# Optimization experiments

Hardware: AMD Instinct MI355X
Metric: run time of the kernel (lower is better)

Reference implementation:

```python
import jax, jax.numpy as jnp
import numpy as np

EMB_SIZE = 50000
D = 256            # emb_dimension
TIMES = 3
D3 = D * TIMES     # 768
RESCALE = 20.0
BATCH = 128
NEG = 5


def setup_inputs() -> dict:
    key = jax.random.key(0)
    ks = jax.random.split(key, 12)
    initrange = 1.0 / D
    return {
        "pos_u": jax.random.randint(ks[0], (BATCH,), 0, EMB_SIZE),
        "pos_v": jax.random.randint(ks[1], (BATCH,), 0, EMB_SIZE),
        "neg_v": jax.random.randint(ks[2], (BATCH, NEG), 0, EMB_SIZE),
        "time": jax.random.uniform(ks[3], (BATCH,), dtype=jnp.float32) * RESCALE,
        "m1": jax.random.normal(ks[4], (1, D), dtype=jnp.float32) / jnp.sqrt(2.0),
        "b1": jax.random.normal(ks[5], (D,), dtype=jnp.float32) * 0.5,
        "W2": jax.random.normal(ks[6], (D, D), dtype=jnp.float32) / jnp.sqrt(D),   # dense2 weight (out,in)
        "b2": jnp.zeros((D,), dtype=jnp.float32),
        "W4": jax.random.normal(ks[7], (D3, D), dtype=jnp.float32) / jnp.sqrt(D),  # dense4 weight (out,in)
        "b4": jnp.zeros((D3,), dtype=jnp.float32),
        "U": jax.random.uniform(ks[8], (EMB_SIZE, D3), dtype=jnp.float32,
                                 minval=-initrange, maxval=initrange),
        "V": jax.random.uniform(ks[9], (EMB_SIZE, D3), dtype=jnp.float32,
                                 minval=-initrange, maxval=initrange),
        "T": jax.random.normal(ks[10], (D, D, D3), dtype=jnp.float32) / D,
        "B": jax.random.normal(ks[11], (D, D), dtype=jnp.float32) / D,
    }


def reference(pos_u, pos_v, neg_v, time, m1, b1, W2, b2, W4, b4, U, V, T, B):
    # time encoding: h1 = tanh(t/rescale * m1 + b1); timevec = tanh(dense2(h1))
    h1 = jnp.tanh((time[:, None] / RESCALE) * m1 + b1)          # (b, d)
    tv = jnp.tanh(h1 @ W2.T + b2)                               # (b, d)
    tvB = tv @ B                                                # einsum('bij,bi->bj') of broadcast B

    # positive target word: (T . emb_u + B) contracted with timevec, then dense4
    emb_u = U[pos_u]                                            # (b, 3d)
    h3_u = jnp.einsum('ijk,bk,bi->bj', T, emb_u, tv) + tvB      # (b, d)
    use_w = h3_u @ W4.T + b4                                    # (b, 3d)

    # positive context word
    emb_v = V[pos_v]                                            # (b, 3d)
    h3_v = jnp.einsum('ijk,bk,bi->bj', T, emb_v, tv) + tvB      # (b, d)
    use_c_v = h3_v @ W4.T + b4                                  # (b, 3d)

    # negative samples: fused contraction avoids the (b, l, d, d) intermediate
    emb_n = V[neg_v]                                            # (b, l, 3d)
    h3_n = jnp.einsum('ijk,blk,bi->blj', T, emb_n, tv) + tvB[:, None, :]  # (b, l, d)
    use_c_n = h3_n @ W4.T + b4                                  # (b, l, 3d)

    score = jnp.sum(use_w * use_c_v, axis=1)
    score = jnp.clip(score, -10.0, 10.0)
    score = -jax.nn.log_sigmoid(score)                          # (b,)

    neg_score = jnp.einsum('blk,bk->bl', use_c_n, use_w)        # bmm with use_w
    neg_score = jnp.clip(neg_score, -10.0, 10.0)
    neg_score = -jnp.mean(jax.nn.log_sigmoid(-neg_score), axis=1)  # (b,)

    return (jnp.mean(score + neg_score), jnp.mean(score), jnp.mean(neg_score))
```

## Files before the change

### kernel.cpp

```cpp
#include <hip/hip_runtime.h>
#include <hip/hip_bf16.h>

#define DD   256
#define DD3  768
#define NB   128
#define NE   7

#define OFF_TVT  0u
#define OFF_TVB  32768u
#define OFF_EMB  65536u
#define OFF_H3   753664u
#define OFF_G    983040u
#define OFF_GV   1048576u
#define OFF_SC   1048832u

typedef __attribute__((ext_vector_type(8))) short bf16x8;
typedef __attribute__((ext_vector_type(4))) float f32x4;

__device__ __forceinline__ unsigned bf16rne(float f) {
  unsigned u = __float_as_uint(f);
  return (u + 0x7fffu + ((u >> 16) & 1u)) >> 16;
}

__device__ __forceinline__ void gld16(const float* g, float* l) {
  __builtin_amdgcn_global_load_lds(
      (const __attribute__((address_space(1))) unsigned int*)g,
      (__attribute__((address_space(3))) unsigned int*)l, 16, 0, 0);
}

__global__ void k_setup(const float* __restrict__ timev,
                        const float* __restrict__ m1,
                        const float* __restrict__ b1,
                        const float* __restrict__ W2,
                        const float* __restrict__ b2,
                        const float* __restrict__ Bm,
                        float* __restrict__ tv_t,
                        float* __restrict__ tvB) {
  const int b = blockIdx.x, i = threadIdx.x;
  __shared__ float h1[DD];
  __shared__ float tvs[DD];
  const float t = timev[b] * (1.0f / 20.0f);
  h1[i] = tanhf(fmaf(t, m1[i], b1[i]));
  __syncthreads();
  float acc = b2[i];
  const float* w2r = W2 + i * DD;
#pragma unroll 8
  for (int jj = 0; jj < DD; ++jj) acc = fmaf(h1[jj], w2r[jj], acc);
  const float tvi = tanhf(acc);
  tvs[i] = tvi;
  tv_t[i * NB + b] = tvi;
  __syncthreads();
  float a2 = 0.f;
#pragma unroll 8
  for (int ii = 0; ii < DD; ++ii) a2 = fmaf(tvs[ii], Bm[ii * DD + i], a2);
  tvB[b * DD + i] = a2;
}

__global__ void k_pack(const float* __restrict__ tv_t, short* __restrict__ tvf) {
  const int t = blockIdx.x * 256 + threadIdx.x;
  const int f = t >> 6, l = t & 63;
  const int b = (f >> 3) * 16 + (l & 15);
  const int i0 = (f & 7) * 32 + ((l >> 4) & 3) * 8;
  bf16x8 v;
#pragma unroll
  for (int jj = 0; jj < 8; ++jj)
    v[jj] = (short)bf16rne(tv_t[(i0 + jj) * NB + b]);
  *(bf16x8*)(tvf + (long)t * 8) = v;
}

__global__ void k_gather(const int* __restrict__ pos_u,
                         const int* __restrict__ pos_v,
                         const int* __restrict__ neg_v,
                         const float* __restrict__ U,
                         const float* __restrict__ V,
                         float* __restrict__ emb) {
  const int be = blockIdx.x;
  const int b = be / NE, e = be % NE;
  const float* src;
  if (e == 0)      src = U + (long)pos_u[b] * DD3;
  else if (e == 1) src = V + (long)pos_v[b] * DD3;
  else             src = V + (long)neg_v[b * 5 + (e - 2)] * DD3;
  const float4 v = ((const float4*)src)[threadIdx.x];
  ((float4*)(emb + ((long)e * NB + b) * DD3))[threadIdx.x] = v;
}

__global__ __launch_bounds__(1024) void k_gram(const float* __restrict__ W4,
                                               const float* __restrict__ b4,
                                               float* __restrict__ G,
                                               float* __restrict__ gv) {
  const int p = blockIdx.x, t = threadIdx.x;
  const int q = t & 255, nq = t >> 8;
  __shared__ float colp[DD3];
  __shared__ float red[4][257];
  __shared__ float gred[4];
  for (int n = t; n < DD3; n += 1024) colp[n] = W4[n * DD + p];
  __syncthreads();
  float acc = 0.f;
  const int n0 = nq * 192;
#pragma unroll 8
  for (int n = n0; n < n0 + 192; ++n) acc = fmaf(colp[n], W4[n * DD + q], acc);
  red[nq][q] = acc;
  float gp = 0.f;
  for (int n = n0; n < n0 + 192; ++n) gp = fmaf(b4[n], colp[n], gp);
  if (q == 0) gred[nq] = gp;
  __syncthreads();
  if (t < 256) G[p * DD + t] = red[0][t] + red[1][t] + red[2][t] + red[3][t];
  if (t == 0) gv[p] = gred[0] + gred[1] + gred[2] + gred[3];
}

__global__ __launch_bounds__(512) void k_main(const float* __restrict__ T,
                                              const short* __restrict__ tvf,
                                              const float* __restrict__ emb,
                                              const float* __restrict__ tvB,
                                              float* __restrict__ h3) {
  __shared__ float Ts[2][4096];
  __shared__ float h3red[NB][NE];
  const int t = threadIdx.x;
  const int j = blockIdx.x;
  const int l = t & 63;
  const int w = t >> 6;
  const int bq = w >> 1;
  const int mh = w & 1;
  const int l15 = l & 15;
  const int l4 = (l >> 4) & 3;
  const int lhi = l >> 5;
  const int kb = (l & 31) * 4;

  bf16x8 tvfr[2][8];
#pragma unroll
  for (int nf = 0; nf < 2; ++nf)
#pragma unroll
    for (int it = 0; it < 8; ++it)
      tvfr[nf][it] = *(const bf16x8*)(tvf + ((((bq * 2 + nf) * 8) + it) * 64 + l) * 8);

  const int i0 = 4 * w + lhi, i1 = i0 + 2;
  const float* gp0 = T + (long)i0 * 196608 + j * 768 + (kb ^ (((i0 >> 3) & 3) << 4));
  const float* gp1 = T + (long)i1 * 196608 + j * 768 + (kb ^ (((i1 >> 3) & 3) << 4));

  auto stage = [&](int kcp, int itp, int bufp) {
    const long o = (long)itp * 6291456 + kcp * 128;
    gld16(gp0 + o, &Ts[bufp][(w * 2 + 0) * 256]);
    gld16(gp1 + o, &Ts[bufp][(w * 2 + 1) * 256]);
  };

  float h3p[NE][2];
#pragma unroll
  for (int e = 0; e < NE; ++e) { h3p[e][0] = 0.f; h3p[e][1] = 0.f; }

  stage(0, 0, 0);
  const int kcol0 = mh * 64;

#pragma unroll 1
  for (int kc = 0; kc < 6; ++kc) {
    f32x4 acc[4][2];
#pragma unroll
    for (int mf = 0; mf < 4; ++mf) {
      acc[mf][0] = {0.f, 0.f, 0.f, 0.f};
      acc[mf][1] = {0.f, 0.f, 0.f, 0.f};
    }
#pragma unroll
    for (int it = 0; it < 8; ++it) {
      if (it < 7) {
        stage(kc, it + 1, (it + 1) & 1);
        asm volatile("s_waitcnt vmcnt(2)" ::: "memory");
      } else if (kc < 5) {
        stage(kc + 1, 0, 0);
        asm volatile("s_waitcnt vmcnt(2)" ::: "memory");
      } else {
        asm volatile("s_waitcnt vmcnt(0)" ::: "memory");
      }
      __builtin_amdgcn_s_barrier();
      asm volatile("" ::: "memory");
      const float* tsb = &Ts[it & 1][0];
#pragma unroll
      for (int mf = 0; mf < 4; ++mf) {
        const int kx = (kcol0 + mf * 16 + l15) ^ (l4 << 4);
        bf16x8 af;
#pragma unroll
        for (int jj = 0; jj < 8; ++jj)
          af[jj] = (short)bf16rne(tsb[(l4 * 8 + jj) * 128 + kx]);
        acc[mf][0] = __builtin_amdgcn_mfma_f32_16x16x32_bf16(af, tvfr[0][it], acc[mf][0], 0, 0, 0);
        acc[mf][1] = __builtin_amdgcn_mfma_f32_16x16x32_bf16(af, tvfr[1][it], acc[mf][1], 0, 0, 0);
      }
      asm volatile("" ::: "memory");
      __builtin_amdgcn_s_barrier();
      asm volatile("" ::: "memory");
    }
#pragma unroll
    for (int nf = 0; nf < 2; ++nf) {
      const int b = bq * 32 + nf * 16 + l15;
#pragma unroll
      for (int mf = 0; mf < 4; ++mf) {
        const long ko = (long)kc * 128 + mh * 64 + mf * 16 + l4 * 4;
#pragma unroll
        for (int e = 0; e < NE; ++e) {
          const f32x4 em = *(const f32x4*)(emb + ((long)e * NB + b) * 768 + ko);
          float s = h3p[e][nf];
          s = fmaf(acc[mf][nf][0], em[0], s);
          s = fmaf(acc[mf][nf][1], em[1], s);
          s = fmaf(acc[mf][nf][2], em[2], s);
          s = fmaf(acc[mf][nf][3], em[3], s);
          h3p[e][nf] = s;
        }
      }
    }
  }

  float hr[NE][2];
#pragma unroll
  for (int e = 0; e < NE; ++e)
#pragma unroll
    for (int nf = 0; nf < 2; ++nf) {
      float v = h3p[e][nf];
      v += __shfl_xor(v, 16);
      v += __shfl_xor(v, 32);
      hr[e][nf] = v;
    }
  __syncthreads();
  if (mh == 0 && l < 16) {
#pragma unroll
    for (int e = 0; e < NE; ++e) {
      h3red[bq * 32 + l][e]      = hr[e][0];
      h3red[bq * 32 + 16 + l][e] = hr[e][1];
    }
  }
  __syncthreads();
  if (mh == 1 && l < 16) {
#pragma unroll
    for (int nf = 0; nf < 2; ++nf) {
      const int b = bq * 32 + nf * 16 + l;
      const float tb = tvB[b * DD + j];
#pragma unroll
      for (int e = 0; e < NE; ++e)
        h3[((long)b * NE + e) * DD + j] = h3red[b][e] + hr[e][nf] + tb;
    }
  }
}

__global__ void k_score(const float* __restrict__ h3,
                        const float* __restrict__ G,
                        const float* __restrict__ gv,
                        const float* __restrict__ b4,
                        float* __restrict__ scoreb,
                        float* __restrict__ negb) {
  const int b = blockIdx.x, t = threadIdx.x;
  __shared__ float h3s[NE * DD];
  __shared__ float red[4][16];
  for (int idx = t; idx < NE * DD; idx += 256) h3s[idx] = h3[(long)b * NE * DD + idx];
  __syncthreads();
  float racc = 0.f;
#pragma unroll 8
  for (int jp = 0; jp < DD; ++jp) racc = fmaf(G[jp * DD + t], h3s[jp], racc);

  float loc[14];
#pragma unroll
  for (int e = 1; e < NE; ++e) loc[e - 1] = racc * h3s[e * DD + t];
  loc[6] = gv[t] * h3s[t];
#pragma unroll
  for (int e = 1; e < NE; ++e) loc[6 + e] = gv[t] * h3s[e * DD + t];
  loc[13] = b4[t] * b4[t] + b4[t + 256] * b4[t + 256] + b4[t + 512] * b4[t + 512];

  const int lane = t & 63, wid = t >> 6;
#pragma unroll
  for (int qd = 0; qd < 14; ++qd) {
    float v = loc[qd];
#pragma unroll
    for (int m = 1; m < 64; m <<= 1) v += __shfl_xor(v, m);
    if (lane == 0) red[wid][qd] = v;
  }
  __syncthreads();
  if (t == 0) {
    float r[14];
#pragma unroll
    for (int qd = 0; qd < 14; ++qd)
      r[qd] = red[0][qd] + red[1][qd] + red[2][qd] + red[3][qd];
    const float c = r[13], gu = r[6];
    auto logsig = [](float x) { return fminf(x, 0.f) - log1pf(expf(-fabsf(x))); };
    float dv = r[0] + gu + r[7] + c;
    dv = fminf(fmaxf(dv, -10.f), 10.f);
    const float sc = -logsig(dv);
    float ns = 0.f;
    for (int lx = 1; lx < 6; ++lx) {
      float dn = r[lx] + gu + r[7 + lx] + c;
      dn = fminf(fmaxf(dn, -10.f), 10.f);
      ns -= logsig(-dn);
    }
    scoreb[b] = sc;
    negb[b] = ns * 0.2f;
  }
}

__global__ void k_final(const float* __restrict__ scoreb,
                        const float* __restrict__ negb,
                        float* __restrict__ out) {
  const int t = threadIdx.x;
  float s = scoreb[t], n = negb[t];
#pragma unroll
  for (int m = 1; m < 64; m <<= 1) {
    s += __shfl_xor(s, m);
    n += __shfl_xor(n, m);
  }
  __shared__ float rs[2], rn[2];
  if ((t & 63) == 0) { rs[t >> 6] = s; rn[t >> 6] = n; }
  __syncthreads();
  if (t == 0) {
    const float S = (rs[0] + rs[1]) * (1.0f / 128.0f);
    const float N = (rn[0] + rn[1]) * (1.0f / 128.0f);
    out[0] = S + N;
    out[1] = S;
    out[2] = N;
  }
}

extern "C" void kernel_launch(void* const* d_in, const int* in_sizes, int n_in,
                              void* d_out, int out_size, void* d_ws, size_t ws_size,
                              hipStream_t stream) {
  const int*   pos_u = (const int*)d_in[0];
  const int*   pos_v = (const int*)d_in[1];
  const int*   neg_v = (const int*)d_in[2];
  const float* timev = (const float*)d_in[3];
  const float* m1    = (const float*)d_in[4];
  const float* b1    = (const float*)d_in[5];
  const float* W2    = (const float*)d_in[6];
  const float* b2    = (const float*)d_in[7];
  const float* W4    = (const float*)d_in[8];
  const float* b4    = (const float*)d_in[9];
  const float* U     = (const float*)d_in[10];
  const float* V     = (const float*)d_in[11];
  const float* T     = (const float*)d_in[12];
  const float* Bm    = (const float*)d_in[13];

  float* ws     = (float*)d_ws;
  float* tv_t   = ws + OFF_TVT;
  float* tvB    = ws + OFF_TVB;
  float* emb    = ws + OFF_EMB;
  float* h3     = ws + OFF_H3;
  float* G      = ws + OFF_G;
  float* gv     = ws + OFF_GV;
  short* tvf    = (short*)(ws + OFF_SC);
  float* scoreb = ws + OFF_SC;
  float* negb   = ws + OFF_SC + 128;
  float* out    = (float*)d_out;

  k_setup<<<128, 256, 0, stream>>>(timev, m1, b1, W2, b2, Bm, tv_t, tvB);
  k_pack<<<16, 256, 0, stream>>>(tv_t, tvf);
  k_gather<<<896, 192, 0, stream>>>(pos_u, pos_v, neg_v, U, V, emb);
  k_gram<<<256, 1024, 0, stream>>>(W4, b4, G, gv);
  k_main<<<256, 512, 0, stream>>>(T, tvf, emb, tvB, h3);
  k_score<<<128, 256, 0, stream>>>(h3, G, gv, b4, scoreb, negb);
  k_final<<<1, 128, 0, stream>>>(scoreb, negb, out);
}
```

Before: 182.5 us.

## Split k_main over batch halves with XCD-aware mapping and deeper staging

k_main now launches 512 blocks. Each block handles one output column j and half of the batch, and block ids are remapped so that blocks sharing a column land on the same XCD and can share L2. The T-slice staging ring grows from 2 to 4 LDS buffers with 3 stages in flight, and MFMA sections are wrapped in s_setprio. The aim is more parallelism and better latency hiding on the T stream. The cost is that each T slice is now read by two blocks instead of one, and LDS use per block rises.

```diff
diff --git a/kernel.cpp b/kernel.cpp
--- a/kernel.cpp
+++ b/kernel.cpp
@@ -113,10 +113,14 @@
                                               const float* __restrict__ emb,
                                               const float* __restrict__ tvB,
                                               float* __restrict__ h3) {
-  __shared__ float Ts[2][4096];
-  __shared__ float h3red[NB][NE];
+  __shared__ float Ts[4][4096];
+  __shared__ float h3red[64][NE];
+  const int bid = blockIdx.x;
+  const int xcd = bid & 7, slot = bid >> 3;
+  const int j = xcd * 32 + (slot >> 1);
+  const int bh = slot & 1;
+
   const int t = threadIdx.x;
-  const int j = blockIdx.x;
   const int l = t & 63;
   const int w = t >> 6;
   const int bq = w >> 1;
@@ -126,114 +130,129 @@
   const int lhi = l >> 5;
   const int kb = (l & 31) * 4;
 
-  bf16x8 tvfr[2][8];
-#pragma unroll
-  for (int nf = 0; nf < 2; ++nf)
-#pragma unroll
-    for (int it = 0; it < 8; ++it)
-      tvfr[nf][it] = *(const bf16x8*)(tvf + ((((bq * 2 + nf) * 8) + it) * 64 + l) * 8);
+  const int bf = bh * 4 + bq;
+  bf16x8 tvfr[8];
+#pragma unroll
+  for (int it = 0; it < 8; ++it)
+    tvfr[it] = *(const bf16x8*)(tvf + (((bf * 8) + it) * 64 + l) * 8);
 
   const int i0 = 4 * w + lhi, i1 = i0 + 2;
   const float* gp0 = T + (long)i0 * 196608 + j * 768 + (kb ^ (((i0 >> 3) & 3) << 4));
   const float* gp1 = T + (long)i1 * 196608 + j * 768 + (kb ^ (((i1 >> 3) & 3) << 4));
 
-  auto stage = [&](int kcp, int itp, int bufp) {
+  auto stage = [&](int sid) {
+    const int itp = sid & 7, kcp = sid >> 3, bufp = sid & 3;
     const long o = (long)itp * 6291456 + kcp * 128;
     gld16(gp0 + o, &Ts[bufp][(w * 2 + 0) * 256]);
     gld16(gp1 + o, &Ts[bufp][(w * 2 + 1) * 256]);
   };
 
-  float h3p[NE][2];
-#pragma unroll
-  for (int e = 0; e < NE; ++e) { h3p[e][0] = 0.f; h3p[e][1] = 0.f; }
-
-  stage(0, 0, 0);
+  float h3p[NE];
+#pragma unroll
+  for (int e = 0; e < NE; ++e) h3p[e] = 0.f;
+
   const int kcol0 = mh * 64;
 
+  auto compute = [&](int buf, int it, f32x4 (&acc)[4]) {
+    const float* tsb = &Ts[buf][0];
+    __builtin_amdgcn_s_setprio(1);
+#pragma unroll
+    for (int mf = 0; mf < 4; ++mf) {
+      const int kx = (kcol0 + mf * 16 + l15) ^ (l4 << 4);
+      bf16x8 af;
+#pragma unroll
+      for (int jj = 0; jj < 8; ++jj)
+        af[jj] = (short)bf16rne(tsb[(l4 * 8 + jj) * 128 + kx]);
+      acc[mf] = __builtin_amdgcn_mfma_f32_16x16x32_bf16(af, tvfr[it], acc[mf], 0, 0, 0);
+    }
+    __builtin_amdgcn_s_setprio(0);
+  };
+
+  auto epilogue = [&](int kc, f32x4 (&acc)[4]) {
+    const int b = bh * 64 + bq * 16 + l15;
+#pragma unroll
+    for (int mf = 0; mf < 4; ++mf) {
+      const long ko = (long)kc * 128 + mh * 64 + mf * 16 + l4 * 4;
+#pragma unroll
+      for (int e = 0; e < NE; ++e) {
+        const f32x4 em = *(const f32x4*)(emb + ((long)e * NB + b) * 768 + ko);
+        float s = h3p[e];
+        s = fmaf(acc[mf][0], em[0], s);
+        s = fmaf(acc[mf][1], em[1], s);
+        s = fmaf(acc[mf][2], em[2], s);
+        s = fmaf(acc[mf][3], em[3], s);
+        h3p[e] = s;
+      }
+    }
+  };
+
+  stage(0); stage(1); stage(2);
+
 #pragma unroll 1
-  for (int kc = 0; kc < 6; ++kc) {
-    f32x4 acc[4][2];
-#pragma unroll
-    for (int mf = 0; mf < 4; ++mf) {
-      acc[mf][0] = {0.f, 0.f, 0.f, 0.f};
-      acc[mf][1] = {0.f, 0.f, 0.f, 0.f};
-    }
+  for (int kc = 0; kc < 5; ++kc) {
+    f32x4 acc[4];
+#pragma unroll
+    for (int mf = 0; mf < 4; ++mf) acc[mf] = {0.f, 0.f, 0.f, 0.f};
 #pragma unroll
     for (int it = 0; it < 8; ++it) {
-      if (it < 7) {
-        stage(kc, it + 1, (it + 1) & 1);
-        asm volatile("s_waitcnt vmcnt(2)" ::: "memory");
-      } else if (kc < 5) {
-        stage(kc + 1, 0, 0);
+      const int sid = kc * 8 + it;
+      stage(sid + 3);
+      asm volatile("s_waitcnt vmcnt(6)" ::: "memory");
+      __builtin_amdgcn_s_barrier();
+      asm volatile("" ::: "memory");
+      compute(sid & 3, it, acc);
+      asm volatile("" ::: "memory");
+      __builtin_amdgcn_s_barrier();
+    }
+    epilogue(kc, acc);
+  }
+  {
+    f32x4 acc[4];
+#pragma unroll
+    for (int mf = 0; mf < 4; ++mf) acc[mf] = {0.f, 0.f, 0.f, 0.f};
+#pragma unroll
+    for (int it = 0; it < 8; ++it) {
+      const int sid = 40 + it;
+      if (it < 5) {
+        stage(sid + 3);
+        asm volatile("s_waitcnt vmcnt(6)" ::: "memory");
+      } else if (it == 5) {
+        asm volatile("s_waitcnt vmcnt(4)" ::: "memory");
+      } else if (it == 6) {
         asm volatile("s_waitcnt vmcnt(2)" ::: "memory");
       } else {
         asm volatile("s_waitcnt vmcnt(0)" ::: "memory");
       }
       __builtin_amdgcn_s_barrier();
       asm volatile("" ::: "memory");
-      const float* tsb = &Ts[it & 1][0];
-#pragma unroll
-      for (int mf = 0; mf < 4; ++mf) {
-        const int kx = (kcol0 + mf * 16 + l15) ^ (l4 << 4);
-        bf16x8 af;
-#pragma unroll
-        for (int jj = 0; jj < 8; ++jj)
-          af[jj] = (short)bf16rne(tsb[(l4 * 8 + jj) * 128 + kx]);
-        acc[mf][0] = __builtin_amdgcn_mfma_f32_16x16x32_bf16(af, tvfr[0][it], acc[mf][0], 0, 0, 0);
-        acc[mf][1] = __builtin_amdgcn_mfma_f32_16x16x32_bf16(af, tvfr[1][it], acc[mf][1], 0, 0, 0);
-      }
+      compute(sid & 3, it, acc);
       asm volatile("" ::: "memory");
       __builtin_amdgcn_s_barrier();
-      asm volatile("" ::: "memory");
-    }
-#pragma unroll
-    for (int nf = 0; nf < 2; ++nf) {
-      const int b = bq * 32 + nf * 16 + l15;
-#pragma unroll
-      for (int mf = 0; mf < 4; ++mf) {
-        const long ko = (long)kc * 128 + mh * 64 + mf * 16 + l4 * 4;
-#pragma unroll
-        for (int e = 0; e < NE; ++e) {
-          const f32x4 em = *(const f32x4*)(emb + ((long)e * NB + b) * 768 + ko);
-          float s = h3p[e][nf];
-          s = fmaf(acc[mf][nf][0], em[0], s);
-          s = fmaf(acc[mf][nf][1], em[1], s);
-          s = fmaf(acc[mf][nf][2], em[2], s);
-          s = fmaf(acc[mf][nf][3], em[3], s);
-          h3p[e][nf] = s;
-        }
-      }
-    }
-  }
-
-  float hr[NE][2];
-#pragma unroll
-  for (int e = 0; e < NE; ++e)
-#pragma unroll
-    for (int nf = 0; nf < 2; ++nf) {
-      float v = h3p[e][nf];
-      v += __shfl_xor(v, 16);
-      v += __shfl_xor(v, 32);
-      hr[e][nf] = v;
-    }
+    }
+    epilogue(5, acc);
+  }
+
+  float hr[NE];
+#pragma unroll
+  for (int e = 0; e < NE; ++e) {
+    float v = h3p[e];
+    v += __shfl_xor(v, 16);
+    v += __shfl_xor(v, 32);
+    hr[e] = v;
+  }
   __syncthreads();
   if (mh == 0 && l < 16) {
 #pragma unroll
-    for (int e = 0; e < NE; ++e) {
-      h3red[bq * 32 + l][e]      = hr[e][0];
-      h3red[bq * 32 + 16 + l][e] = hr[e][1];
-    }
+    for (int e = 0; e < NE; ++e) h3red[bq * 16 + l][e] = hr[e];
   }
   __syncthreads();
   if (mh == 1 && l < 16) {
-#pragma unroll
-    for (int nf = 0; nf < 2; ++nf) {
-      const int b = bq * 32 + nf * 16 + l;
-      const float tb = tvB[b * DD + j];
-#pragma unroll
-      for (int e = 0; e < NE; ++e)
-        h3[((long)b * NE + e) * DD + j] = h3red[b][e] + hr[e][nf] + tb;
-    }
+    const int bl = bq * 16 + l;
+    const int b = bh * 64 + bl;
+    const float tb = tvB[b * DD + j];
+#pragma unroll
+    for (int e = 0; e < NE; ++e)
+      h3[((long)b * NE + e) * DD + j] = h3red[bl][e] + hr[e] + tb;
   }
 }
 
@@ -346,7 +365,7 @@
   k_pack<<<16, 256, 0, stream>>>(tv_t, tvf);
   k_gather<<<896, 192, 0, stream>>>(pos_u, pos_v, neg_v, U, V, emb);
   k_gram<<<256, 1024, 0, stream>>>(W4, b4, G, gv);
-  k_main<<<256, 512, 0, stream>>>(T, tvf, emb, tvB, h3);
+  k_main<<<512, 512, 0, stream>>>(T, tvf, emb, tvB, h3);
   k_score<<<128, 256, 0, stream>>>(h3, G, gv, b4, scoreb, negb);
   k_final<<<1, 128, 0, stream>>>(scoreb, negb, out);
 }
```

Result: slower. 213.4 us (+16.9%).

## Split k_main over k-chunks across blocks with atomic reduction and triple buffering

Applied to the files above, without the earlier changes.

The k-chunk loop in k_main becomes a grid dimension, so 1536 blocks each handle one 128-wide k slice instead of 256 blocks looping over six. This raises parallelism across the MI355X CUs for the large T-streaming contraction. Partial h3 results are combined with atomicAdd into a buffer zeroed by a hipMemsetAsync, and tvB is added only by the kc==0 block. The kernel also switches to a three-stage LDS prefetch pipeline, raises MFMA wave priority with s_setprio, and adds a min-blocks launch bound. The costs are atomic contention, an extra memset launch, nondeterministic float summation order, and more LDS per block.

```diff
diff --git a/kernel.cpp b/kernel.cpp
--- a/kernel.cpp
+++ b/kernel.cpp
@@ -108,15 +108,18 @@
   if (t == 0) gv[p] = gred[0] + gred[1] + gred[2] + gred[3];
 }
 
-__global__ __launch_bounds__(512) void k_main(const float* __restrict__ T,
-                                              const short* __restrict__ tvf,
-                                              const float* __restrict__ emb,
-                                              const float* __restrict__ tvB,
-                                              float* __restrict__ h3) {
-  __shared__ float Ts[2][4096];
+__global__ __launch_bounds__(512, 4) void k_main(const float* __restrict__ T,
+                                                 const short* __restrict__ tvf,
+                                                 const float* __restrict__ emb,
+                                                 const float* __restrict__ tvB,
+                                                 float* __restrict__ h3) {
+  __shared__ float Ts[3][4096];
   __shared__ float h3red[NB][NE];
+  const int bid = blockIdx.x;
+  const int j = bid & 255;
+  const int kc = bid >> 8;
+
   const int t = threadIdx.x;
-  const int j = blockIdx.x;
   const int l = t & 63;
   const int w = t >> 6;
   const int bq = w >> 1;
@@ -134,74 +137,75 @@
       tvfr[nf][it] = *(const bf16x8*)(tvf + ((((bq * 2 + nf) * 8) + it) * 64 + l) * 8);
 
   const int i0 = 4 * w + lhi, i1 = i0 + 2;
-  const float* gp0 = T + (long)i0 * 196608 + j * 768 + (kb ^ (((i0 >> 3) & 3) << 4));
-  const float* gp1 = T + (long)i1 * 196608 + j * 768 + (kb ^ (((i1 >> 3) & 3) << 4));
-
-  auto stage = [&](int kcp, int itp, int bufp) {
-    const long o = (long)itp * 6291456 + kcp * 128;
-    gld16(gp0 + o, &Ts[bufp][(w * 2 + 0) * 256]);
-    gld16(gp1 + o, &Ts[bufp][(w * 2 + 1) * 256]);
+  const float* gp0 = T + (long)i0 * 196608 + j * 768 + kc * 128 + (kb ^ (((i0 >> 3) & 3) << 4));
+  const float* gp1 = T + (long)i1 * 196608 + j * 768 + kc * 128 + (kb ^ (((i1 >> 3) & 3) << 4));
+
+  auto stage = [&](int it) {
+    const int buf = it % 3;
+    const long o = (long)it * 6291456;
+    gld16(gp0 + o, &Ts[buf][(w * 2 + 0) * 256]);
+    gld16(gp1 + o, &Ts[buf][(w * 2 + 1) * 256]);
   };
 
+  const int kcol0 = mh * 64;
+
+  f32x4 acc[4][2];
+#pragma unroll
+  for (int mf = 0; mf < 4; ++mf) {
+    acc[mf][0] = {0.f, 0.f, 0.f, 0.f};
+    acc[mf][1] = {0.f, 0.f, 0.f, 0.f};
+  }
+
+  stage(0); stage(1);
+
+#pragma unroll
+  for (int it = 0; it < 8; ++it) {
+    if (it < 6) {
+      stage(it + 2);
+      asm volatile("s_waitcnt vmcnt(4)" ::: "memory");
+    } else if (it == 6) {
+      asm volatile("s_waitcnt vmcnt(2)" ::: "memory");
+    } else {
+      asm volatile("s_waitcnt vmcnt(0)" ::: "memory");
+    }
+    __builtin_amdgcn_s_barrier();
+    asm volatile("" ::: "memory");
+    const float* tsb = &Ts[it % 3][0];
+    __builtin_amdgcn_s_setprio(1);
+#pragma unroll
+    for (int mf = 0; mf < 4; ++mf) {
+      const int kx = (kcol0 + mf * 16 + l15) ^ (l4 << 4);
+      bf16x8 af;
+#pragma unroll
+      for (int jj = 0; jj < 8; ++jj)
+        af[jj] = (short)bf16rne(tsb[(l4 * 8 + jj) * 128 + kx]);
+      acc[mf][0] = __builtin_amdgcn_mfma_f32_16x16x32_bf16(af, tvfr[0][it], acc[mf][0], 0, 0, 0);
+      acc[mf][1] = __builtin_amdgcn_mfma_f32_16x16x32_bf16(af, tvfr[1][it], acc[mf][1], 0, 0, 0);
+    }
+    __builtin_amdgcn_s_setprio(0);
+    asm volatile("" ::: "memory");
+    __builtin_amdgcn_s_barrier();
+    asm volatile("" ::: "memory");
+  }
+
   float h3p[NE][2];
 #pragma unroll
   for (int e = 0; e < NE; ++e) { h3p[e][0] = 0.f; h3p[e][1] = 0.f; }
-
-  stage(0, 0, 0);
-  const int kcol0 = mh * 64;
-
-#pragma unroll 1
-  for (int kc = 0; kc < 6; ++kc) {
-    f32x4 acc[4][2];
+#pragma unroll
+  for (int nf = 0; nf < 2; ++nf) {
+    const int b = bq * 32 + nf * 16 + l15;
 #pragma unroll
     for (int mf = 0; mf < 4; ++mf) {
-      acc[mf][0] = {0.f, 0.f, 0.f, 0.f};
-      acc[mf][1] = {0.f, 0.f, 0.f, 0.f};
-    }
-#pragma unroll
-    for (int it = 0; it < 8; ++it) {
-      if (it < 7) {
-        stage(kc, it + 1, (it + 1) & 1);
-        asm volatile("s_waitcnt vmcnt(2)" ::: "memory");
-      } else if (kc < 5) {
-        stage(kc + 1, 0, 0);
-        asm volatile("s_waitcnt vmcnt(2)" ::: "memory");
-      } else {
-        asm volatile("s_waitcnt vmcnt(0)" ::: "memory");
-      }
-      __builtin_amdgcn_s_barrier();
-      asm volatile("" ::: "memory");
-      const float* tsb = &Ts[it & 1][0];
-#pragma unroll
-      for (int mf = 0; mf < 4; ++mf) {
-        const int kx = (kcol0 + mf * 16 + l15) ^ (l4 << 4);
-        bf16x8 af;
-#pragma unroll
-        for (int jj = 0; jj < 8; ++jj)
-          af[jj] = (short)bf16rne(tsb[(l4 * 8 + jj) * 128 + kx]);
-        acc[mf][0] = __builtin_amdgcn_mfma_f32_16x16x32_bf16(af, tvfr[0][it], acc[mf][0], 0, 0, 0);
-        acc[mf][1] = __builtin_amdgcn_mfma_f32_16x16x32_bf16(af, tvfr[1][it], acc[mf][1], 0, 0, 0);
-      }
-      asm volatile("" ::: "memory");
-      __builtin_amdgcn_s_barrier();
-      asm volatile("" ::: "memory");
-    }
-#pragma unroll
-    for (int nf = 0; nf < 2; ++nf) {
-      const int b = bq * 32 + nf * 16 + l15;
-#pragma unroll
-      for (int mf = 0; mf < 4; ++mf) {
-        const long ko = (long)kc * 128 + mh * 64 + mf * 16 + l4 * 4;
-#pragma unroll
-        for (int e = 0; e < NE; ++e) {
-          const f32x4 em = *(const f32x4*)(emb + ((long)e * NB + b) * 768 + ko);
-          float s = h3p[e][nf];
-          s = fmaf(acc[mf][nf][0], em[0], s);
-          s = fmaf(acc[mf][nf][1], em[1], s);
-          s = fmaf(acc[mf][nf][2], em[2], s);
-          s = fmaf(acc[mf][nf][3], em[3], s);
-          h3p[e][nf] = s;
-        }
+      const long ko = (long)kc * 128 + mh * 64 + mf * 16 + l4 * 4;
+#pragma unroll
+      for (int e = 0; e < NE; ++e) {
+        const f32x4 em = *(const f32x4*)(emb + ((long)e * NB + b) * 768 + ko);
+        float s = h3p[e][nf];
+        s = fmaf(acc[mf][nf][0], em[0], s);
+        s = fmaf(acc[mf][nf][1], em[1], s);
+        s = fmaf(acc[mf][nf][2], em[2], s);
+        s = fmaf(acc[mf][nf][3], em[3], s);
+        h3p[e][nf] = s;
       }
     }
   }
@@ -229,10 +233,10 @@
 #pragma unroll
     for (int nf = 0; nf < 2; ++nf) {
       const int b = bq * 32 + nf * 16 + l;
-      const float tb = tvB[b * DD + j];
+      const float tb = (kc == 0) ? tvB[b * DD + j] : 0.f;
 #pragma unroll
       for (int e = 0; e < NE; ++e)
-        h3[((long)b * NE + e) * DD + j] = h3red[b][e] + hr[e][nf] + tb;
+        atomicAdd(&h3[((long)b * NE + e) * DD + j], h3red[b][e] + hr[e][nf] + tb);
     }
   }
 }
@@ -342,11 +346,12 @@
   float* negb   = ws + OFF_SC + 128;
   float* out    = (float*)d_out;
 
+  hipMemsetAsync(h3, 0, (size_t)NB * NE * DD * sizeof(float), stream);
   k_setup<<<128, 256, 0, stream>>>(timev, m1, b1, W2, b2, Bm, tv_t, tvB);
   k_pack<<<16, 256, 0, stream>>>(tv_t, tvf);
   k_gather<<<896, 192, 0, stream>>>(pos_u, pos_v, neg_v, U, V, emb);
   k_gram<<<256, 1024, 0, stream>>>(W4, b4, G, gv);
-  k_main<<<256, 512, 0, stream>>>(T, tvf, emb, tvB, h3);
+  k_main<<<1536, 512, 0, stream>>>(T, tvf, emb, tvB, h3);
   k_score<<<128, 256, 0, stream>>>(h3, G, gv, b4, scoreb, negb);
   k_final<<<1, 128, 0, stream>>>(scoreb, negb, out);
 }
```

Measured after the change: 205.5 us. 1.13x slower.
